# Performance work log

Measured on AMD Instinct MI355X. Metric: run time of the kernel, lower is better.

Reference implementation:

```python
import jax, jax.numpy as jnp
import numpy as np

E = 2  # expand_ratio


def _linear_scan(u, a):
    """h_t = a_t * h_{t-1} + u_t along axis 0, h_{-1}=0. Parallel associative scan."""
    def comb(x, y):
        a1, b1 = x
        a2, b2 = y
        return a2 * a1, a2 * b1 + b2
    _, h = jax.lax.associative_scan(comb, (a, u), axis=0)
    return h


def setup_inputs() -> dict:
    key = jax.random.key(0)
    ks = jax.random.split(key, 8)
    n, b, d = 2048, 4, 1024
    s = 1.0 / np.sqrt(d)
    return {
        "x": jax.random.normal(ks[0], (n, b, d), jnp.float32),
        "lower_bound": jax.random.uniform(ks[1], (d,), jnp.float32),
        "W_in": jax.random.normal(ks[2], (d, 3 * d), jnp.float32) * s,
        "b_in": jnp.zeros((3 * d,), jnp.float32),
        "W_out": jax.random.normal(ks[3], (d, d), jnp.float32) * s,
        "b_out": jnp.zeros((d,), jnp.float32),
        "gamma": jnp.ones((d,), jnp.float32),
        "beta": jnp.zeros((d,), jnp.float32),
    }


def reference(x, lower_bound, W_in, b_in, W_out, b_out, gamma, beta):
    n, b, d = x.shape
    h = d // E
    feat = x @ W_in + b_in                      # (n,b,3d)
    inp, og, fg = jnp.split(feat, 3, axis=-1)
    inp = jax.nn.silu(inp)
    og = jax.nn.sigmoid(og)
    fg = jax.nn.sigmoid(fg)
    # reshape (h d) -> h, d=E
    inp = inp.reshape(n, b, h, E)
    og = og.reshape(n, b, h, E)
    fg = fg.reshape(n, b, h, E)
    lb = lower_bound.reshape(h, E)
    lam = lb + (1.0 - lb) * fg                  # (n,b,h,E)
    # outer-product input: (1-lam) outer inp over the E dims -> (n,b,h,E,E)
    u = jnp.einsum('nbhd,nbhe->nbhde', 1.0 - lam, inp)
    a = jnp.broadcast_to(lam[..., None], u.shape)
    u = u.reshape(n, b, h * E * E)
    a = a.reshape(n, b, h * E * E)
    state_fwd = _linear_scan(u, a)
    state_rev = jnp.flip(_linear_scan(jnp.flip(u, 0), jnp.flip(a, 0)), 0)
    state = (state_fwd + state_rev).reshape(n, b, h, E, E)
    out = jnp.einsum('nbhde,nbhd->nbhe', state, og).reshape(n, b, d)
    # layernorm over last dim
    mu = jnp.mean(out, axis=-1, keepdims=True)
    var = jnp.var(out, axis=-1, keepdims=True)
    out = (out - mu) * jax.lax.rsqrt(var + 1e-5) * gamma + beta
    return out @ W_out + b_out
```

## Files before the change

### kernel.cpp

```cpp
#include <hip/hip_runtime.h>

typedef __bf16 bf16x8 __attribute__((ext_vector_type(8)));
typedef float floatx4 __attribute__((ext_vector_type(4)));

#define NCH 128
#define CLEN 16

__device__ __forceinline__ unsigned short f2bf(float f) {
  unsigned int u = __builtin_bit_cast(unsigned int, f);
  u += 0x7fff + ((u >> 16) & 1);
  return (unsigned short)(u >> 16);
}
__device__ __forceinline__ float bf2f(unsigned short u) {
  unsigned int v = (unsigned int)u << 16;
  return __builtin_bit_cast(float, v);
}
__device__ __forceinline__ float bf2f_lo(unsigned int u) {
  return __builtin_bit_cast(float, u << 16);
}
__device__ __forceinline__ float bf2f_hi(unsigned int u) {
  return __builtin_bit_cast(float, u & 0xffff0000u);
}

__device__ __forceinline__ void async_copy16(const void* g, void* l) {
  __builtin_amdgcn_global_load_lds(
      (const __attribute__((address_space(1))) unsigned int*)g,
      (__attribute__((address_space(3))) unsigned int*)l, 16, 0, 0);
}

__device__ __forceinline__ bf16x8 ds_read16(unsigned addr) {
  bf16x8 r;
  asm volatile("ds_read_b128 %0, %1" : "=v"(r) : "v"(addr));
  return r;
}

__global__ void cast_x_kernel(const float* __restrict__ in, unsigned short* __restrict__ out) {
  int i = blockIdx.x * blockDim.x + threadIdx.x;
  float4 v = ((const float4*)in)[i];
  ushort4 o;
  o.x = f2bf(v.x); o.y = f2bf(v.y); o.z = f2bf(v.z); o.w = f2bf(v.w);
  ((ushort4*)out)[i] = o;
}

__global__ void tcast2_kernel(const float* __restrict__ Win, unsigned short* __restrict__ winT,
                              const float* __restrict__ Wout, unsigned short* __restrict__ woutT) {
  __shared__ float tile[32][33];
  int bx = blockIdx.x;
  const float* W;
  unsigned short* WT;
  int ncols, n0;
  if (bx < 96) { W = Win; WT = winT; ncols = 3072; n0 = bx * 32; }
  else { W = Wout; WT = woutT; ncols = 1024; n0 = (bx - 96) * 32; }
  int k0 = blockIdx.y * 32;
  int tx = threadIdx.x, ty = threadIdx.y;
  tile[ty][tx] = W[(size_t)(k0 + ty) * ncols + n0 + tx];
  __syncthreads();
  WT[(size_t)(n0 + ty) * 1024 + k0 + tx] = f2bf(tile[tx][ty]);
}

template <int EPI>
__global__ __launch_bounds__(256) void gemm_kernel(
    const unsigned short* __restrict__ A, const unsigned short* __restrict__ BT,
    const float* __restrict__ bias, const float* __restrict__ lb,
    float* __restrict__ outf,
    unsigned short* __restrict__ o_inp, unsigned short* __restrict__ o_og,
    unsigned short* __restrict__ o_om) {
  __shared__ alignas(16) char smem_raw[17408];
  unsigned short* As = (unsigned short*)smem_raw;
  unsigned short* Bs = As + 128 * 32;
  const int m0 = blockIdx.x * 128, n0 = blockIdx.y * 128;
  const int tid = threadIdx.x;
  const int lane = tid & 63, wave = tid >> 6;
  const int wm = (wave >> 1) * 64, wn = (wave & 1) * 64;
  const int mrow = lane & 15, q = lane >> 4;
  const int qsw = q ^ ((mrow >> 1) & 3);
  floatx4 acc[4][4] = {};
  const int r0 = wave * 32;
  const int srow = r0 + (lane >> 2);
  const int qs = (lane & 3) ^ ((srow >> 1) & 3);
  const unsigned short* gA0 = A + (size_t)(m0 + srow) * 1024 + qs * 8;
  const unsigned short* gA1 = gA0 + (size_t)16 * 1024;
  const unsigned short* gB0 = BT + (size_t)(n0 + srow) * 1024 + qs * 8;
  const unsigned short* gB1 = gB0 + (size_t)16 * 1024;
  unsigned short* lA0 = &As[r0 * 32];
  unsigned short* lA1 = &As[(r0 + 16) * 32];
  unsigned short* lB0 = &Bs[r0 * 32];
  unsigned short* lB1 = &Bs[(r0 + 16) * 32];
  for (int kt = 0; kt < 1024; kt += 32) {
    __syncthreads();
    async_copy16(gA0, lA0);
    async_copy16(gA1, lA1);
    async_copy16(gB0, lB0);
    async_copy16(gB1, lB1);
    gA0 += 32; gA1 += 32; gB0 += 32; gB1 += 32;
    __syncthreads();
    bf16x8 af[4], bf[4];
#pragma unroll
    for (int i = 0; i < 4; i++) af[i] = *(const bf16x8*)&As[(wm + i * 16 + mrow) * 32 + qsw * 8];
#pragma unroll
    for (int j = 0; j < 4; j++) bf[j] = *(const bf16x8*)&Bs[(wn + j * 16 + mrow) * 32 + qsw * 8];
#pragma unroll
    for (int i = 0; i < 4; i++)
#pragma unroll
      for (int j = 0; j < 4; j++)
        acc[i][j] = __builtin_amdgcn_mfma_f32_16x16x32_bf16(af[i], bf[j], acc[i][j], 0, 0, 0);
  }
  const int er = tid >> 3;
  const int ec = (tid & 7) * 16;
  const int rgbase = m0 + (er & 15) + (er >> 4) * 64;
  const int lr = (wm ? 16 : 0) + q * 4;
  float bi[4];
  int cidx[4];
#pragma unroll
  for (int j = 0; j < 4; j++) {
    cidx[j] = n0 + wn + j * 16 + mrow;
    bi[j] = bias[cidx[j]];
  }
  if (EPI == 1) {
    unsigned short* Cs = (unsigned short*)smem_raw;
    const int seg = n0 >> 10;
    unsigned short* dst = (seg == 0) ? o_inp : (seg == 1) ? o_og : o_om;
    float Lv[4];
    if (seg == 2) {
#pragma unroll
      for (int j = 0; j < 4; j++) Lv[j] = lb[cidx[j] & 1023];
    }
#pragma unroll
    for (int i = 0; i < 4; i++) {
      __syncthreads();
#pragma unroll
      for (int j = 0; j < 4; j++) {
        const int lc = wn + j * 16 + mrow;
#pragma unroll
        for (int g = 0; g < 4; g++) {
          float v = acc[i][j][g] + bi[j];
          unsigned short ob;
          if (seg == 0) { float s = 1.f / (1.f + __expf(-v)); ob = f2bf(v * s); }
          else if (seg == 1) { float s = 1.f / (1.f + __expf(-v)); ob = f2bf(s); }
          else { float sm = 1.f / (1.f + __expf(v)); ob = f2bf((1.f - Lv[j]) * sm); }
          Cs[(lr + g) * 136 + lc] = ob;
        }
      }
      __syncthreads();
      uint4 v0 = *(uint4*)&Cs[er * 136 + ec];
      uint4 v1 = *(uint4*)&Cs[er * 136 + ec + 8];
      size_t ro = (size_t)(rgbase + i * 16) * 1024 + (n0 & 1023) + ec;
      *(uint4*)&dst[ro] = v0;
      *(uint4*)&dst[ro + 8] = v1;
    }
  } else {
    float* Cf = (float*)smem_raw;
#pragma unroll
    for (int i = 0; i < 4; i++) {
      __syncthreads();
#pragma unroll
      for (int j = 0; j < 4; j++) {
        const int lc = wn + j * 16 + mrow;
#pragma unroll
        for (int g = 0; g < 4; g++) Cf[(lr + g) * 132 + lc] = acc[i][j][g] + bi[j];
      }
      __syncthreads();
      size_t ro = (size_t)(rgbase + i * 16) * 1024 + n0 + ec;
#pragma unroll
      for (int k = 0; k < 4; k++) {
        float4 v = *(float4*)&Cf[er * 132 + ec + k * 4];
        *(float4*)&outf[ro + k * 4] = v;
      }
    }
  }
}

__global__ __launch_bounds__(512, 2) void gemm1_kernel(
    const unsigned short* __restrict__ A, const unsigned short* __restrict__ BT,
    const float* __restrict__ bias, const float* __restrict__ lb,
    unsigned short* __restrict__ o_inp, unsigned short* __restrict__ o_og,
    unsigned short* __restrict__ o_om) {
  __shared__ alignas(16) char smem[131072];
  const int orig = blockIdx.x;
  const int wg = (orig & 7) * 48 + (orig >> 3);
  const int m0 = (wg / 12) << 8;
  const int n0 = (wg % 12) << 8;
  const int tid = threadIdx.x;
  const int lane = tid & 63, wave = tid >> 6;
  const int wm = wave >> 2, wn = wave & 3;
  const int srow = tid >> 3;
  const int sq = (tid & 7) ^ (srow & 7);
  const unsigned short* gA = A + (size_t)(m0 + srow) * 1024 + sq * 8;
  const unsigned short* gB = BT + (size_t)(n0 + srow) * 1024 + sq * 8;
  char* lw = smem + wave * 1024;
  const int aro = (wm * 128 + (lane & 15)) * 128;
  const int bro = (wn * 64 + (lane & 15)) * 128;
  const int qs0 = ((lane >> 4) ^ (lane & 7)) * 16;
  const int qs1 = ((4 + (lane >> 4)) ^ (lane & 7)) * 16;
  const unsigned sbase = (unsigned)(size_t)(void*)smem;
  const unsigned aA[2][2] = {{sbase + 0 + aro + qs0, sbase + 0 + aro + qs1},
                             {sbase + 32768 + aro + qs0, sbase + 32768 + aro + qs1}};
  const unsigned aB[2][2] = {{sbase + 65536 + bro + qs0, sbase + 65536 + bro + qs1},
                             {sbase + 98304 + bro + qs0, sbase + 98304 + bro + qs1}};

  floatx4 acc[8][4] = {};
  bf16x8 aF[4][2], bF[4][2];

#define STG(lofs, gh, kk)                                \
  do {                                                   \
    const unsigned short* _g = (gh) + (size_t)(kk) * 64; \
    async_copy16(_g, lw + (lofs));                       \
    async_copy16(_g + 65536, lw + (lofs) + 8192);        \
  } while (0)
#define RA(buf, mh, i, s) ds_read16(aA[buf][s] + (mh) * 8192 + (i) * 2048)
#define RB(buf, j, s) ds_read16(aB[buf][s] + (j) * 2048)
#define BAR __builtin_amdgcn_s_barrier()
#define LGKM0 do { asm volatile("s_waitcnt lgkmcnt(0)" ::: "memory"); \
                   __builtin_amdgcn_sched_barrier(0); } while (0)
#define VM4 asm volatile("s_waitcnt vmcnt(4)" ::: "memory")
#define VM8 asm volatile("s_waitcnt vmcnt(8)" ::: "memory")
#define MM(d, a, b) d = __builtin_amdgcn_mfma_f32_16x16x32_bf16(a, b, d, 0, 0, 0)

  STG(65536, gB, 0);
  STG(65536 + 16384, gB + 131072, 0);
  STG(0, gA, 0);
  STG(16384, gA + 131072, 0);
  STG(98304, gB, 1);
  STG(98304 + 16384, gB + 131072, 1);
  STG(32768, gA, 1);
  STG(32768 + 16384, gA + 131072, 1);
  VM8;
  BAR;

#pragma unroll 1
  for (int it = 0; it < 8; ++it) {
    const int t0 = 2 * it;
    const int kN2 = (t0 + 2 > 15) ? 15 : t0 + 2;
    const int kN3 = (t0 + 3 > 15) ? 15 : t0 + 3;
#pragma unroll
    for (int i = 0; i < 4; i++) { aF[i][0] = RA(0, 0, i, 0); aF[i][1] = RA(0, 0, i, 1); }
#pragma unroll
    for (int j = 0; j < 2; j++) { bF[j][0] = RB(0, j, 0); bF[j][1] = RB(0, j, 1); }
    BAR; LGKM0;
    __builtin_amdgcn_s_setprio(1);
#pragma unroll
    for (int i = 0; i < 4; i++)
#pragma unroll
      for (int j = 0; j < 2; j++) { MM(acc[i][j], aF[i][0], bF[j][0]); MM(acc[i][j], aF[i][1], bF[j][1]); }
    __builtin_amdgcn_s_setprio(0);
    BAR;
#pragma unroll
    for (int j = 2; j < 4; j++) { bF[j][0] = RB(0, j, 0); bF[j][1] = RB(0, j, 1); }
    BAR; LGKM0;
    __builtin_amdgcn_s_setprio(1);
#pragma unroll
    for (int i = 0; i < 4; i++)
#pragma unroll
      for (int j = 2; j < 4; j++) { MM(acc[i][j], aF[i][0], bF[j][0]); MM(acc[i][j], aF[i][1], bF[j][1]); }
    __builtin_amdgcn_s_setprio(0);
    BAR;
#pragma unroll
    for (int i = 0; i < 4; i++) { aF[i][0] = RA(0, 1, i, 0); aF[i][1] = RA(0, 1, i, 1); }
    STG(65536, gB, kN2);
    STG(65536 + 16384, gB + 131072, kN2);
    BAR; LGKM0;
    __builtin_amdgcn_s_setprio(1);
#pragma unroll
    for (int i = 0; i < 4; i++)
#pragma unroll
      for (int j = 0; j < 2; j++) { MM(acc[4 + i][j], aF[i][0], bF[j][0]); MM(acc[4 + i][j], aF[i][1], bF[j][1]); }
    __builtin_amdgcn_s_setprio(0);
    BAR;
    STG(0, gA, kN2);
    STG(16384, gA + 131072, kN2);
    BAR;
    __builtin_amdgcn_s_setprio(1);
#pragma unroll
    for (int i = 0; i < 4; i++)
#pragma unroll
      for (int j = 2; j < 4; j++) { MM(acc[4 + i][j], aF[i][0], bF[j][0]); MM(acc[4 + i][j], aF[i][1], bF[j][1]); }
    __builtin_amdgcn_s_setprio(0);
    VM4;
    BAR;
#pragma unroll
    for (int i = 0; i < 4; i++) { aF[i][0] = RA(1, 0, i, 0); aF[i][1] = RA(1, 0, i, 1); }
#pragma unroll
    for (int j = 0; j < 2; j++) { bF[j][0] = RB(1, j, 0); bF[j][1] = RB(1, j, 1); }
    BAR; LGKM0;
    __builtin_amdgcn_s_setprio(1);
#pragma unroll
    for (int i = 0; i < 4; i++)
#pragma unroll
      for (int j = 0; j < 2; j++) { MM(acc[i][j], aF[i][0], bF[j][0]); MM(acc[i][j], aF[i][1], bF[j][1]); }
    __builtin_amdgcn_s_setprio(0);
    BAR;
#pragma unroll
    for (int j = 2; j < 4; j++) { bF[j][0] = RB(1, j, 0); bF[j][1] = RB(1, j, 1); }
    BAR; LGKM0;
    __builtin_amdgcn_s_setprio(1);
#pragma unroll
    for (int i = 0; i < 4; i++)
#pragma unroll
      for (int j = 2; j < 4; j++) { MM(acc[i][j], aF[i][0], bF[j][0]); MM(acc[i][j], aF[i][1], bF[j][1]); }
    __builtin_amdgcn_s_setprio(0);
    BAR;
#pragma unroll
    for (int i = 0; i < 4; i++) { aF[i][0] = RA(1, 1, i, 0); aF[i][1] = RA(1, 1, i, 1); }
    STG(98304, gB, kN3);
    STG(98304 + 16384, gB + 131072, kN3);
    BAR; LGKM0;
    __builtin_amdgcn_s_setprio(1);
#pragma unroll
    for (int i = 0; i < 4; i++)
#pragma unroll
      for (int j = 0; j < 2; j++) { MM(acc[4 + i][j], aF[i][0], bF[j][0]); MM(acc[4 + i][j], aF[i][1], bF[j][1]); }
    __builtin_amdgcn_s_setprio(0);
    BAR;
    STG(32768, gA, kN3);
    STG(32768 + 16384, gA + 131072, kN3);
    BAR;
    __builtin_amdgcn_s_setprio(1);
#pragma unroll
    for (int i = 0; i < 4; i++)
#pragma unroll
      for (int j = 2; j < 4; j++) { MM(acc[4 + i][j], aF[i][0], bF[j][0]); MM(acc[4 + i][j], aF[i][1], bF[j][1]); }
    __builtin_amdgcn_s_setprio(0);
    VM4;
    BAR;
  }
#undef STG
#undef RA
#undef RB
#undef BAR
#undef LGKM0
#undef VM4
#undef VM8
#undef MM

  asm volatile("s_waitcnt vmcnt(0) lgkmcnt(0)" ::: "memory");
  const int seg = n0 >> 10;
  unsigned short* dst = (seg == 0) ? o_inp : (seg == 1) ? o_og : o_om;
  unsigned short* Cs = (unsigned short*)smem;
  float bi[4], Lv[4];
#pragma unroll
  for (int j = 0; j < 4; j++) {
    const int c = n0 + wn * 64 + j * 16 + (lane & 15);
    bi[j] = bias[c];
    Lv[j] = (seg == 2) ? lb[c & 1023] : 0.f;
  }
  const int lrw = wm * 16 + (lane >> 4) * 4;
  const int lcw = wn * 64 + (lane & 15);
  const int er = tid >> 4, ec = (tid & 15) * 16;
  const int growb = m0 + (er >> 4) * 128 + (er & 15);
#pragma unroll
  for (int i = 0; i < 8; i++) {
    __syncthreads();
#pragma unroll
    for (int j = 0; j < 4; j++)
#pragma unroll
      for (int g = 0; g < 4; g++) {
        float v = acc[i][j][g] + bi[j];
        unsigned short ob;
        if (seg == 0) { float s = 1.f / (1.f + __expf(-v)); ob = f2bf(v * s); }
        else if (seg == 1) { float s = 1.f / (1.f + __expf(-v)); ob = f2bf(s); }
        else { float sm = 1.f / (1.f + __expf(v)); ob = f2bf((1.f - Lv[j]) * sm); }
        Cs[(lrw + g) * 264 + lcw + j * 16] = ob;
      }
    __syncthreads();
    uint4 v0 = *(uint4*)&Cs[er * 264 + ec];
    uint4 v1 = *(uint4*)&Cs[er * 264 + ec + 8];
    size_t ro = (size_t)(growb + i * 16) * 1024 + (n0 & 1023) + ec;
    *(uint4*)&dst[ro] = v0;
    *(uint4*)&dst[ro + 8] = v1;
  }
}

__global__ void scan_passA(const unsigned short* __restrict__ om, const unsigned short* __restrict__ ip,
                           float* __restrict__ sumA, float* __restrict__ sumBf,
                           float* __restrict__ sumBr) {
  int idx = blockIdx.x * 256 + threadIdx.x;
  int h = idx & 511, cb = idx >> 9, b = cb & 3, c = cb >> 2;
  long base = ((long)c * CLEN * 4 + b) * 1024 + 2 * h;
  float p0 = 1.f, p1 = 1.f;
  float s00 = 0.f, s01 = 0.f, s10 = 0.f, s11 = 0.f;
  float r00 = 0.f, r01 = 0.f, r10 = 0.f, r11 = 0.f;
#pragma unroll
  for (int t = 0; t < CLEN; t++) {
    ushort2 l2 = *(const ushort2*)(om + base);
    ushort2 i2 = *(const ushort2*)(ip + base);
    base += 4096;
    float omx = bf2f(l2.x), omy = bf2f(l2.y);
    float ipx = bf2f(i2.x), ipy = bf2f(i2.y);
    float lx = 1.f - omx, ly = 1.f - omy;
    float u00 = omx * ipx, u01 = omx * ipy, u10 = omy * ipx, u11 = omy * ipy;
    r00 += p0 * u00; r01 += p0 * u01; r10 += p1 * u10; r11 += p1 * u11;
    s00 = lx * s00 + u00; s01 = lx * s01 + u01;
    s10 = ly * s10 + u10; s11 = ly * s11 + u11;
    p0 *= lx; p1 *= ly;
  }
  ((float2*)sumA)[idx] = make_float2(p0, p1);
  ((float4*)sumBf)[idx] = make_float4(s00, s01, s10, s11);
  ((float4*)sumBr)[idx] = make_float4(r00, r01, r10, r11);
}

__global__ void scan_passB(const float* __restrict__ sumA, const float* __restrict__ sumBf,
                           const float* __restrict__ sumBr, float* __restrict__ initF,
                           float* __restrict__ initR) {
  int tid = blockIdx.x * 256 + threadIdx.x;
  int dir = tid >> 13;
  int rem = tid & 8191;
  int ch = rem & 3;
  int bh = rem >> 2;
  int dd = ch >> 1;
  if (dir == 0) {
    float H = 0.f;
    for (int c = 0; c < NCH; c++) {
      int si = c * 2048 + bh;
      initF[(size_t)si * 4 + ch] = H;
      H = sumA[(size_t)si * 2 + dd] * H + sumBf[(size_t)si * 4 + ch];
    }
  } else {
    float G = 0.f;
    for (int c = NCH - 1; c >= 0; c--) {
      int si = c * 2048 + bh;
      initR[(size_t)si * 4 + ch] = G;
      G = sumA[(size_t)si * 2 + dd] * G + sumBr[(size_t)si * 4 + ch];
    }
  }
}

__global__ __launch_bounds__(512) void scanC_ln_kernel(
    const unsigned short* __restrict__ om, const unsigned short* __restrict__ ip,
    const unsigned short* __restrict__ og,
    const float* __restrict__ initF, const float* __restrict__ initR,
    const float* __restrict__ gamma, const float* __restrict__ beta,
    unsigned short* __restrict__ ybf) {
  __shared__ float tile[8][1024];
  __shared__ float ldsG[1024];
  __shared__ float ldsB[1024];
  const int h = threadIdx.x;
  const int cb = blockIdx.x;
  const int b = cb & 3, c = cb >> 2;
  const int idx = cb * 512 + h;
  *(float2*)&ldsG[2 * h] = *(const float2*)(gamma + 2 * h);
  *(float2*)&ldsB[2 * h] = *(const float2*)(beta + 2 * h);
  float4 F = ((const float4*)initF)[idx];
  float4 R = ((const float4*)initR)[idx];
  float outx[CLEN], outy[CLEN];
  unsigned int lS[CLEN], iS[CLEN], oS[CLEN];
  const long base = ((long)c * CLEN * 4 + b) * 1024 + 2 * h;
  float h00 = F.x, h01 = F.y, h10 = F.z, h11 = F.w;
  long p = base;
#pragma unroll
  for (int t = 0; t < CLEN; t++) {
    unsigned int l2 = *(const unsigned int*)(om + p);
    unsigned int i2 = *(const unsigned int*)(ip + p);
    unsigned int o2 = *(const unsigned int*)(og + p);
    p += 4096;
    lS[t] = l2; iS[t] = i2; oS[t] = o2;
    float omx = bf2f_lo(l2), omy = bf2f_hi(l2);
    float ipx = bf2f_lo(i2), ipy = bf2f_hi(i2);
    float ox = bf2f_lo(o2), oy = bf2f_hi(o2);
    float lx = 1.f - omx, ly = 1.f - omy;
    h00 = lx * h00 + omx * ipx; h01 = lx * h01 + omx * ipy;
    h10 = ly * h10 + omy * ipx; h11 = ly * h11 + omy * ipy;
    outx[t] = h00 * ox + h10 * oy;
    outy[t] = h01 * ox + h11 * oy;
  }
  float g00 = R.x, g01 = R.y, g10 = R.z, g11 = R.w;
#pragma unroll
  for (int t = CLEN - 1; t >= 0; t--) {
    unsigned int l2 = lS[t], i2 = iS[t], o2 = oS[t];
    float omx = bf2f_lo(l2), omy = bf2f_hi(l2);
    float ipx = bf2f_lo(i2), ipy = bf2f_hi(i2);
    float ox = bf2f_lo(o2), oy = bf2f_hi(o2);
    float lx = 1.f - omx, ly = 1.f - omy;
    g00 = omx * ipx + lx * g00; g01 = omx * ipy + lx * g01;
    g10 = omy * ipx + ly * g10; g11 = omy * ipy + ly * g11;
    outx[t] += g00 * ox + g10 * oy;
    outy[t] += g01 * ox + g11 * oy;
  }
  const int lane = h & 63, wv = h >> 6;
#pragma unroll
  for (int g = 0; g < CLEN / 8; g++) {
    __syncthreads();
#pragma unroll
    for (int r = 0; r < 8; r++) {
      float2 v2 = make_float2(outx[g * 8 + r], outy[g * 8 + r]);
      *(float2*)&tile[r][2 * h] = v2;
    }
    __syncthreads();
    {
      const int t = g * 8 + wv;
      float4 v[4];
#pragma unroll
      for (int k = 0; k < 4; k++) v[k] = *(const float4*)&tile[wv][lane * 16 + k * 4];
      float s = 0.f, s2 = 0.f;
#pragma unroll
      for (int k = 0; k < 4; k++) {
        s += v[k].x + v[k].y + v[k].z + v[k].w;
        s2 += v[k].x * v[k].x + v[k].y * v[k].y + v[k].z * v[k].z + v[k].w * v[k].w;
      }
#pragma unroll
      for (int off = 1; off < 64; off <<= 1) {
        s += __shfl_xor(s, off);
        s2 += __shfl_xor(s2, off);
      }
      float mean = s * (1.f / 1024.f);
      float var = s2 * (1.f / 1024.f) - mean * mean;
      float rstd = rsqrtf(var + 1e-5f);
      unsigned short o16[16];
#pragma unroll
      for (int k = 0; k < 4; k++) {
        float* vv = (float*)&v[k];
#pragma unroll
        for (int e = 0; e < 4; e++) {
          int ch = lane * 16 + k * 4 + e;
          o16[k * 4 + e] = f2bf((vv[e] - mean) * rstd * ldsG[ch] + ldsB[ch]);
        }
      }
      size_t rowo = ((size_t)(c * CLEN + t) * 4 + b) * 1024 + lane * 16;
      *(uint4*)(ybf + rowo) = *(uint4*)&o16[0];
      *(uint4*)(ybf + rowo + 8) = *(uint4*)&o16[8];
    }
  }
}

extern "C" void kernel_launch(void* const* d_in, const int* in_sizes, int n_in,
                              void* d_out, int out_size, void* d_ws, size_t ws_size,
                              hipStream_t stream) {
  const float* x = (const float*)d_in[0];
  const float* lb = (const float*)d_in[1];
  const float* Win = (const float*)d_in[2];
  const float* bin = (const float*)d_in[3];
  const float* Wout = (const float*)d_in[4];
  const float* bout = (const float*)d_in[5];
  const float* gamma = (const float*)d_in[6];
  const float* beta = (const float*)d_in[7];
  float* out = (float*)d_out;

  char* ws = (char*)d_ws;
  size_t off = 0;
  auto alloc = [&](size_t bytes) {
    void* p = ws + off;
    off += (bytes + 255) & ~(size_t)255;
    return p;
  };
  unsigned short* x_bf = (unsigned short*)alloc(8192ull * 1024 * 2);
  unsigned short* winT = (unsigned short*)alloc(3072ull * 1024 * 2);
  unsigned short* woutT = (unsigned short*)alloc(1024ull * 1024 * 2);
  unsigned short* inp_b = (unsigned short*)alloc(8192ull * 1024 * 2);
  unsigned short* og_b = (unsigned short*)alloc(8192ull * 1024 * 2);
  unsigned short* om_b = (unsigned short*)alloc(8192ull * 1024 * 2);
  unsigned short* y_bf = (unsigned short*)alloc(8192ull * 1024 * 2);
  float* sumA = (float*)alloc((size_t)NCH * 4 * 512 * 2 * 4);
  float* sumBf = (float*)alloc((size_t)NCH * 4 * 512 * 4 * 4);
  float* sumBr = (float*)alloc((size_t)NCH * 4 * 512 * 4 * 4);
  float* initF = (float*)alloc((size_t)NCH * 4 * 512 * 4 * 4);
  float* initR = (float*)alloc((size_t)NCH * 4 * 512 * 4 * 4);

  cast_x_kernel<<<8192, 256, 0, stream>>>(x, x_bf);
  tcast2_kernel<<<dim3(128, 32), dim3(32, 32), 0, stream>>>(Win, winT, Wout, woutT);
  gemm1_kernel<<<384, 512, 0, stream>>>(x_bf, winT, bin, lb, inp_b, og_b, om_b);
  scan_passA<<<(NCH * 4 * 512) / 256, 256, 0, stream>>>(om_b, inp_b, sumA, sumBf, sumBr);
  scan_passB<<<64, 256, 0, stream>>>(sumA, sumBf, sumBr, initF, initR);
  scanC_ln_kernel<<<NCH * 4, 512, 0, stream>>>(om_b, inp_b, og_b, initF, initR, gamma, beta, y_bf);
  gemm_kernel<0><<<dim3(64, 8), 256, 0, stream>>>(y_bf, woutT, bout, nullptr, out, nullptr, nullptr, nullptr);
}
```

Measured before the change: 264.6 us.

## Overlap LDS fragment reads with MFMA via partial lgkmcnt waits in GEMM loop

Restructures the main GEMM loop schedule so LDS fragment reads are issued earlier and consumed with partial lgkmcnt waits (8/4/0) instead of full waits. MFMA groups start as soon as their operands land, and B fragments for the next stage are prefetched across the phase boundary. It also reorders the vmcnt waits and drops one barrier per phase. This aims to hide LDS latency and cut barrier stalls, but it relies on the in-order lgkm counting being correct and raises register pressure.

```diff
diff --git a/kernel.cpp b/kernel.cpp
--- a/kernel.cpp
+++ b/kernel.cpp
@@ -209,12 +209,46 @@
   } while (0)
 #define RA(buf, mh, i, s) ds_read16(aA[buf][s] + (mh) * 8192 + (i) * 2048)
 #define RB(buf, j, s) ds_read16(aB[buf][s] + (j) * 2048)
+#define ISSUE_A(buf, mh)                                           \
+  do {                                                             \
+    aF[0][0] = RA(buf, mh, 0, 0); aF[0][1] = RA(buf, mh, 0, 1);    \
+    aF[1][0] = RA(buf, mh, 1, 0); aF[1][1] = RA(buf, mh, 1, 1);    \
+    aF[2][0] = RA(buf, mh, 2, 0); aF[2][1] = RA(buf, mh, 2, 1);    \
+    aF[3][0] = RA(buf, mh, 3, 0); aF[3][1] = RA(buf, mh, 3, 1);    \
+  } while (0)
+#define ISSUE_B01(buf)                                   \
+  do {                                                   \
+    bF[0][0] = RB(buf, 0, 0); bF[0][1] = RB(buf, 0, 1);  \
+    bF[1][0] = RB(buf, 1, 0); bF[1][1] = RB(buf, 1, 1);  \
+  } while (0)
+#define ISSUE_B23(buf)                                   \
+  do {                                                   \
+    bF[2][0] = RB(buf, 2, 0); bF[2][1] = RB(buf, 2, 1);  \
+    bF[3][0] = RB(buf, 3, 0); bF[3][1] = RB(buf, 3, 1);  \
+  } while (0)
 #define BAR __builtin_amdgcn_s_barrier()
-#define LGKM0 do { asm volatile("s_waitcnt lgkmcnt(0)" ::: "memory"); \
-                   __builtin_amdgcn_sched_barrier(0); } while (0)
-#define VM4 asm volatile("s_waitcnt vmcnt(4)" ::: "memory")
-#define VM8 asm volatile("s_waitcnt vmcnt(8)" ::: "memory")
+#define LGKM(n)                                                   \
+  do {                                                            \
+    asm volatile("s_waitcnt lgkmcnt(" #n ")" ::: "memory");       \
+    __builtin_amdgcn_sched_barrier(0);                            \
+  } while (0)
+#define VM8                                                       \
+  do {                                                            \
+    asm volatile("s_waitcnt vmcnt(8)" ::: "memory");              \
+    __builtin_amdgcn_sched_barrier(0);                            \
+  } while (0)
 #define MM(d, a, b) d = __builtin_amdgcn_mfma_f32_16x16x32_bf16(a, b, d, 0, 0, 0)
+#define MMC(ab, I0, I1, J0, J1)                              \
+  do {                                                       \
+    __builtin_amdgcn_s_setprio(1);                           \
+    _Pragma("unroll") for (int _i = (I0); _i < (I1); _i++) { \
+      _Pragma("unroll") for (int _j = (J0); _j < (J1); _j++) {\
+        MM(acc[(ab) + _i][_j], aF[_i][0], bF[_j][0]);        \
+        MM(acc[(ab) + _i][_j], aF[_i][1], bF[_j][1]);        \
+      }                                                      \
+    }                                                        \
+    __builtin_amdgcn_s_setprio(0);                           \
+  } while (0)
 
   STG(65536, gB, 0);
   STG(65536 + 16384, gB + 131072, 0);
@@ -226,111 +260,79 @@
   STG(32768 + 16384, gA + 131072, 1);
   VM8;
   BAR;
+  ISSUE_B01(0);
 
 #pragma unroll 1
   for (int it = 0; it < 8; ++it) {
     const int t0 = 2 * it;
     const int kN2 = (t0 + 2 > 15) ? 15 : t0 + 2;
     const int kN3 = (t0 + 3 > 15) ? 15 : t0 + 3;
-#pragma unroll
-    for (int i = 0; i < 4; i++) { aF[i][0] = RA(0, 0, i, 0); aF[i][1] = RA(0, 0, i, 1); }
-#pragma unroll
-    for (int j = 0; j < 2; j++) { bF[j][0] = RB(0, j, 0); bF[j][1] = RB(0, j, 1); }
-    BAR; LGKM0;
-    __builtin_amdgcn_s_setprio(1);
-#pragma unroll
-    for (int i = 0; i < 4; i++)
-#pragma unroll
-      for (int j = 0; j < 2; j++) { MM(acc[i][j], aF[i][0], bF[j][0]); MM(acc[i][j], aF[i][1], bF[j][1]); }
-    __builtin_amdgcn_s_setprio(0);
-    BAR;
-#pragma unroll
-    for (int j = 2; j < 4; j++) { bF[j][0] = RB(0, j, 0); bF[j][1] = RB(0, j, 1); }
-    BAR; LGKM0;
-    __builtin_amdgcn_s_setprio(1);
-#pragma unroll
-    for (int i = 0; i < 4; i++)
-#pragma unroll
-      for (int j = 2; j < 4; j++) { MM(acc[i][j], aF[i][0], bF[j][0]); MM(acc[i][j], aF[i][1], bF[j][1]); }
-    __builtin_amdgcn_s_setprio(0);
-    BAR;
-#pragma unroll
-    for (int i = 0; i < 4; i++) { aF[i][0] = RA(0, 1, i, 0); aF[i][1] = RA(0, 1, i, 1); }
+    ISSUE_A(0, 0);
+    ISSUE_B23(0);
+    BAR;
+    LGKM(8);
+    MMC(0, 0, 2, 0, 2);
+    LGKM(4);
+    MMC(0, 2, 4, 0, 2);
+    BAR;
+    LGKM(0);
+    MMC(0, 0, 4, 2, 4);
+    BAR;
+    ISSUE_A(0, 1);
     STG(65536, gB, kN2);
     STG(65536 + 16384, gB + 131072, kN2);
-    BAR; LGKM0;
-    __builtin_amdgcn_s_setprio(1);
-#pragma unroll
-    for (int i = 0; i < 4; i++)
-#pragma unroll
-      for (int j = 0; j < 2; j++) { MM(acc[4 + i][j], aF[i][0], bF[j][0]); MM(acc[4 + i][j], aF[i][1], bF[j][1]); }
-    __builtin_amdgcn_s_setprio(0);
+    BAR;
+    LGKM(4);
+    MMC(4, 0, 2, 0, 2);
+    LGKM(0);
+    MMC(4, 2, 4, 0, 2);
     BAR;
     STG(0, gA, kN2);
     STG(16384, gA + 131072, kN2);
-    BAR;
-    __builtin_amdgcn_s_setprio(1);
-#pragma unroll
-    for (int i = 0; i < 4; i++)
-#pragma unroll
-      for (int j = 2; j < 4; j++) { MM(acc[4 + i][j], aF[i][0], bF[j][0]); MM(acc[4 + i][j], aF[i][1], bF[j][1]); }
-    __builtin_amdgcn_s_setprio(0);
-    VM4;
-    BAR;
-#pragma unroll
-    for (int i = 0; i < 4; i++) { aF[i][0] = RA(1, 0, i, 0); aF[i][1] = RA(1, 0, i, 1); }
-#pragma unroll
-    for (int j = 0; j < 2; j++) { bF[j][0] = RB(1, j, 0); bF[j][1] = RB(1, j, 1); }
-    BAR; LGKM0;
-    __builtin_amdgcn_s_setprio(1);
-#pragma unroll
-    for (int i = 0; i < 4; i++)
-#pragma unroll
-      for (int j = 0; j < 2; j++) { MM(acc[i][j], aF[i][0], bF[j][0]); MM(acc[i][j], aF[i][1], bF[j][1]); }
-    __builtin_amdgcn_s_setprio(0);
-    BAR;
-#pragma unroll
-    for (int j = 2; j < 4; j++) { bF[j][0] = RB(1, j, 0); bF[j][1] = RB(1, j, 1); }
-    BAR; LGKM0;
-    __builtin_amdgcn_s_setprio(1);
-#pragma unroll
-    for (int i = 0; i < 4; i++)
-#pragma unroll
-      for (int j = 2; j < 4; j++) { MM(acc[i][j], aF[i][0], bF[j][0]); MM(acc[i][j], aF[i][1], bF[j][1]); }
-    __builtin_amdgcn_s_setprio(0);
-    BAR;
-#pragma unroll
-    for (int i = 0; i < 4; i++) { aF[i][0] = RA(1, 1, i, 0); aF[i][1] = RA(1, 1, i, 1); }
+    VM8;
+    BAR;
+    ISSUE_B01(1);
+    MMC(4, 0, 4, 2, 4);
+    BAR;
+    ISSUE_A(1, 0);
+    ISSUE_B23(1);
+    BAR;
+    LGKM(8);
+    MMC(0, 0, 2, 0, 2);
+    LGKM(4);
+    MMC(0, 2, 4, 0, 2);
+    BAR;
+    LGKM(0);
+    MMC(0, 0, 4, 2, 4);
+    BAR;
+    ISSUE_A(1, 1);
     STG(98304, gB, kN3);
     STG(98304 + 16384, gB + 131072, kN3);
-    BAR; LGKM0;
-    __builtin_amdgcn_s_setprio(1);
-#pragma unroll
-    for (int i = 0; i < 4; i++)
-#pragma unroll
-      for (int j = 0; j < 2; j++) { MM(acc[4 + i][j], aF[i][0], bF[j][0]); MM(acc[4 + i][j], aF[i][1], bF[j][1]); }
-    __builtin_amdgcn_s_setprio(0);
+    BAR;
+    LGKM(4);
+    MMC(4, 0, 2, 0, 2);
+    LGKM(0);
+    MMC(4, 2, 4, 0, 2);
     BAR;
     STG(32768, gA, kN3);
     STG(32768 + 16384, gA + 131072, kN3);
-    BAR;
-    __builtin_amdgcn_s_setprio(1);
-#pragma unroll
-    for (int i = 0; i < 4; i++)
-#pragma unroll
-      for (int j = 2; j < 4; j++) { MM(acc[4 + i][j], aF[i][0], bF[j][0]); MM(acc[4 + i][j], aF[i][1], bF[j][1]); }
-    __builtin_amdgcn_s_setprio(0);
-    VM4;
+    VM8;
+    BAR;
+    ISSUE_B01(0);
+    MMC(4, 0, 4, 2, 4);
     BAR;
   }
 #undef STG
 #undef RA
 #undef RB
+#undef ISSUE_A
+#undef ISSUE_B01
+#undef ISSUE_B23
 #undef BAR
-#undef LGKM0
-#undef VM4
+#undef LGKM
 #undef VM8
 #undef MM
+#undef MMC
 
   asm volatile("s_waitcnt vmcnt(0) lgkmcnt(0)" ::: "memory");
   const int seg = n0 >> 10;
```

Result: slower. 280.6 us (+6.1%).
